# Kernel optimization log

Measured on AMD Instinct MI355X. Metric: run time of the kernel, lower is better.

## Reference

```python
import jax, jax.numpy as jnp
import numpy as np

B, T, E, D, OUT = 128, 64, 256, 256, 1  # batch, timesteps, encoder_hidden, decoder_hidden, out_feats


def setup_inputs() -> dict:
    key = jax.random.key(0)
    ks = jax.random.split(key, 14)
    s = 0.05
    return {
        "input_encoded": jax.random.normal(ks[0], (B, T, E), jnp.float32),
        "y_history": jax.random.normal(ks[1], (B, T - 1, OUT), jnp.float32),
        # attn_layer: Linear(2D+E -> E), Tanh, Linear(E -> 1)
        "W_a1": jax.random.normal(ks[2], (E, 2 * D + E), jnp.float32) * s,
        "b_a1": jax.random.normal(ks[3], (E,), jnp.float32) * s,
        "W_a2": jax.random.normal(ks[4], (1, E), jnp.float32) * s,
        "b_a2": jax.random.normal(ks[5], (1,), jnp.float32) * s,
        # fc: Linear(E + out_feats -> out_feats)
        "W_fc": jax.random.normal(ks[6], (OUT, E + OUT), jnp.float32) * s,
        "b_fc": jax.random.normal(ks[7], (OUT,), jnp.float32) * s,
        # LSTM(input_size=out_feats, hidden_size=D), gate order i,f,g,o
        "W_ih": jax.random.normal(ks[8], (4 * D, OUT), jnp.float32) * s,
        "W_hh": jax.random.normal(ks[9], (4 * D, D), jnp.float32) * s,
        "b_ih": jax.random.normal(ks[10], (4 * D,), jnp.float32) * s,
        "b_hh": jax.random.normal(ks[11], (4 * D,), jnp.float32) * s,
        # fc_final: Linear(D + E -> 2) (probabilistic=True)
        "W_ff": jax.random.normal(ks[12], (2, D + E), jnp.float32) * s,
        "b_ff": jax.random.normal(ks[13], (2,), jnp.float32) * s,
    }


def reference(input_encoded, y_history, W_a1, b_a1, W_a2, b_a2, W_fc, b_fc,
              W_ih, W_hh, b_ih, b_hh, W_ff, b_ff):
    Bn, Tn, En = input_encoded.shape
    Dn = W_hh.shape[1]

    def step(carry, y_t):
        h, c, _ = carry  # h, c: [B, D]
        # concat(hidden, cell, enc) broadcast over the T encoder positions -> [B, T, 2D+E]
        feats = jnp.concatenate([
            jnp.broadcast_to(h[:, None, :], (Bn, Tn, Dn)),
            jnp.broadcast_to(c[:, None, :], (Bn, Tn, Dn)),
            input_encoded,
        ], axis=2)
        scores = jnp.tanh(feats @ W_a1.T + b_a1) @ W_a2.T + b_a2  # [B, T, 1]
        attn = jax.nn.softmax(scores[..., 0], axis=1)              # [B, T]
        context = jnp.einsum('bt,bte->be', attn, input_encoded)   # [B, E]
        y_tilde = jnp.concatenate([context, y_t], axis=1) @ W_fc.T + b_fc  # [B, 1]
        # single LSTM step, PyTorch gate order (i, f, g, o)
        gates = y_tilde @ W_ih.T + b_ih + h @ W_hh.T + b_hh       # [B, 4D]
        i, f, g, o = jnp.split(gates, 4, axis=1)
        c_new = jax.nn.sigmoid(f) * c + jax.nn.sigmoid(i) * jnp.tanh(g)
        h_new = jax.nn.sigmoid(o) * jnp.tanh(c_new)
        return (h_new, c_new, context), None

    h0 = jnp.zeros((Bn, Dn), input_encoded.dtype)
    c0 = jnp.zeros((Bn, Dn), input_encoded.dtype)
    ctx0 = jnp.zeros((Bn, En), input_encoded.dtype)
    # data_integration=True: loop runs T-1 steps over y_history
    (h, c, context), _ = jax.lax.scan(step, (h0, c0, ctx0), jnp.swapaxes(y_history, 0, 1))
    return jnp.concatenate([h, context], axis=1) @ W_ff.T + b_ff  # [B, 2]
```

## Files before the change

kernel.cpp:

```cpp
#include <hip/hip_runtime.h>
#include <math.h>

#define BATCH 128
#define TENC  64
#define NSTEP 63

#define OFF_WA1ET  0
#define OFF_EPT    65536
#define OFF_PKH    2162688
#define OFF_SX     2359296
#define OFF_HX     2375680
#define OFF_FLAGS  2408448

typedef __attribute__((ext_vector_type(8))) _Float16 h8_t;
typedef __attribute__((ext_vector_type(2))) _Float16 h2_t;

#if defined(__has_builtin)
#if __has_builtin(__builtin_amdgcn_fdot2)
#define FDOT2(a, b, c) __builtin_amdgcn_fdot2((a), (b), (c), false)
#endif
#endif
#ifndef FDOT2
#define FDOT2(a, b, c) ((c) + (float)(a)[0] * (float)(b)[0] + (float)(a)[1] * (float)(b)[1])
#endif

__device__ __forceinline__ h2_t h2of(h8_t v, int i) {
    h2_t r = {v[2 * i], v[2 * i + 1]};
    return r;
}
__device__ __forceinline__ float ftanh(float x) {
    x = fminf(15.f, fmaxf(-15.f, x));
    float e = __expf(2.f * x);
    return (e - 1.f) * __builtin_amdgcn_rcpf(e + 1.f);
}
__device__ __forceinline__ float fsig(float x) {
    return __builtin_amdgcn_rcpf(1.f + __expf(-x));
}
__device__ __forceinline__ unsigned pack_hc(float h, float c) {
    unsigned short hu = __builtin_bit_cast(unsigned short, (_Float16)h);
    unsigned short cu = __builtin_bit_cast(unsigned short, (_Float16)c);
    return (unsigned)hu | ((unsigned)cu << 16);
}

__global__ void pack_weights(const float* __restrict__ Wa1,
                             const float* __restrict__ Whh,
                             float* __restrict__ ws) {
    int idx = blockIdx.x * blockDim.x + threadIdx.x;
    _Float16* PKH = (_Float16*)(ws + OFF_PKH);
    if (idx < 131072) {
        int m = idx & 7, j7 = (idx >> 3) & 127, it = (idx >> 10) & 3;
        int seg = (idx >> 12) & 1, kc = (idx >> 13) & 7, hp = (idx >> 16) & 1;
        int owner = seg ? (1 - hp) : hp;
        int idx256 = kc * 32 + it * 8 + m;
        int k = (idx256 < 128) ? owner * 128 + idx256
                               : 256 + owner * 128 + (idx256 - 128);
        int j = hp * 128 + j7;
        PKH[idx] = (_Float16)Wa1[j * 768 + k];
    } else if (idx < 393216) {
        int n = idx - 131072;
        int m = n & 7, qp = (n >> 3) & 511, kh = (n >> 12) & 1, kk = (n >> 13) & 15, h1 = n >> 17;
        int q = ((qp >> 7) << 8) + h1 * 128 + (qp & 127);
        int k = kh * 128 + kk * 8 + m;
        PKH[131072 + n] = (_Float16)Whh[q * 256 + k];
    } else if (idx < 458752) {
        int n = idx - 393216;
        int k = n >> 8, j = n & 255;
        ws[OFF_WA1ET + n] = Wa1[j * 768 + 512 + k];
    }
}

__global__ void zero_flags(float* __restrict__ ws) {
    unsigned* f = (unsigned*)(ws + OFF_FLAGS);
    f[threadIdx.x] = 0u;
}

__global__ void enc_proj_kernel(const float* __restrict__ enc,
                                const float* __restrict__ ba1,
                                float* __restrict__ ws) {
    __shared__ float smem[8448];
    const int b  = blockIdx.x >> 1;
    const int th = blockIdx.x & 1;
    const int t0 = th * 32;
    const int tid = threadIdx.x;

    const float* encb = enc + (b * TENC + t0) * 256;
    for (int c = 0; c < 32; ++c) smem[c * 256 + tid] = encb[c * 256 + tid];
    __syncthreads();

    const int w = tid >> 6, l = tid & 63;
    float acc[8][4];
    #pragma unroll
    for (int a = 0; a < 8; ++a)
        #pragma unroll
        for (int c = 0; c < 4; ++c) acc[a][c] = 0.f;

    const float4* WT = (const float4*)(ws + OFF_WA1ET);
    for (int k = 0; k < 256; ++k) {
        float4 wv = WT[k * 64 + l];
        #pragma unroll
        for (int tt = 0; tt < 8; ++tt) {
            float e = smem[(w * 8 + tt) * 256 + k];
            acc[tt][0] += e * wv.x; acc[tt][1] += e * wv.y;
            acc[tt][2] += e * wv.z; acc[tt][3] += e * wv.w;
        }
    }
    float4 bb = ((const float4*)ba1)[l];
    __syncthreads();
    #pragma unroll
    for (int tt = 0; tt < 8; ++tt) {
        smem[(4 * l + 0) * 33 + w * 8 + tt] = acc[tt][0] + bb.x;
        smem[(4 * l + 1) * 33 + w * 8 + tt] = acc[tt][1] + bb.y;
        smem[(4 * l + 2) * 33 + w * 8 + tt] = acc[tt][2] + bb.z;
        smem[(4 * l + 3) * 33 + w * 8 + tt] = acc[tt][3] + bb.w;
    }
    __syncthreads();
    float* EPT = ws + OFF_EPT + b * 16384;
    for (int c = 0; c < 32; ++c) {
        int i = c * 256 + tid;
        int j = i >> 5, t5 = i & 31;
        EPT[j * 64 + t0 + t5] = smem[j * 33 + t5];
    }
}

__global__ __launch_bounds__(1024, 4) void decoder_main(
    const float* __restrict__ enc, const float* __restrict__ yhist,
    const float* __restrict__ Wa2,
    const float* __restrict__ Wfc, const float* __restrict__ bfc,
    const float* __restrict__ wih, const float* __restrict__ bih,
    const float* __restrict__ bhh,
    const float* __restrict__ Wff, const float* __restrict__ bff,
    float* __restrict__ ws, float* __restrict__ out) {

    __shared__ float hc[512];
    __shared__ _Float16 hcf16[512] __attribute__((aligned(16)));
    __shared__ float z[128];
    __shared__ float red1[1024];
    __shared__ float red2[1024];
    __shared__ float g2[1024];
    __shared__ float attnw[64];
    __shared__ float encw[64];
    __shared__ float sownl[64];
    __shared__ float wa2s[128];
    __shared__ float ys[64];
    __shared__ h8_t  wc[6144] __attribute__((aligned(16)));
    __shared__ float epl[8192];

    const int bid  = blockIdx.x;
    const int b    = bid & 127;
    const int h1   = bid >> 7;
    const int tid  = threadIdx.x;
    const int lane = tid & 63;
    const int wv   = tid >> 6;

    const _Float16* PKH = (const _Float16*)(ws + OFF_PKH);

    const float* EPTb = ws + OFF_EPT + b * 16384 + h1 * 8192;
    const float* encb = enc + b * 16384;
    #pragma unroll
    for (int i = 0; i < 8; ++i) epl[i * 1024 + tid] = EPTb[i * 1024 + tid];
    const h8_t* PKGown = (const h8_t*)(PKH + 131072) + h1 * 16384;
    #pragma unroll
    for (int kk = 0; kk < 6; ++kk) wc[kk * 1024 + tid] = PKGown[kk * 1024 + tid];
    if (tid < 512) { hc[tid] = 0.f; hcf16[tid] = (_Float16)0.f; }
    if (tid < 128) wa2s[tid] = Wa2[h1 * 128 + tid];
    if (tid < NSTEP) ys[tid] = yhist[b * NSTEP + tid];
    const float bfc0  = bfc[0];
    const float wfc_y = Wfc[256];
    float wii = 0.f, wif = 0.f, wig = 0.f, wio = 0.f;
    float bsi = 0.f, bsf = 0.f, bsg = 0.f, bso = 0.f;
    if (tid < 128) {
        const int q0 = h1 * 128 + tid;
        wii = wih[q0];       bsi = bih[q0]       + bhh[q0];
        wif = wih[256 + q0]; bsf = bih[256 + q0] + bhh[256 + q0];
        wig = wih[512 + q0]; bsg = bih[512 + q0] + bhh[512 + q0];
        wio = wih[768 + q0]; bso = bih[768 + q0] + bhh[768 + q0];
    }
    {
        const int t = tid >> 4, cch = tid & 15;
        float p = 0.f;
        #pragma unroll
        for (int i = 0; i < 16; ++i)
            p += encb[t * 256 + cch * 16 + i] * Wfc[cch * 16 + i];
        red1[t * 16 + cch] = p;
    }
    __syncthreads();
    if (tid < 64) {
        float s = 0.f;
        #pragma unroll
        for (int c = 0; c < 16; ++c) s += red1[tid * 16 + c];
        encw[tid] = s;
    }
    __syncthreads();

    const int kc = tid >> 7, j7 = tid & 127;
    const h8_t* W1 = (const h8_t*)PKH + h1 * 8192 + kc * 1024 + j7;
    const _Float16* hb_own  = hcf16 + ((kc < 4) ? h1 * 128 + kc * 32
                                                : 256 + h1 * 128 + (kc - 4) * 32);
    const _Float16* hb_peer = hcf16 + ((kc < 4) ? (1 - h1) * 128 + kc * 32
                                                : 256 + (1 - h1) * 128 + (kc - 4) * 32);
    const int kh = tid >> 9, qp = tid & 511;
    const h8_t* W4 = PKGown + kh * 512 + qp;
    const _Float16* hgk = hcf16 + kh * 128;

    float*    SXown  = ws + OFF_SX + (b * 2 + h1) * 64;
    float*    SXpeer = ws + OFF_SX + (b * 2 + (1 - h1)) * 64;
    unsigned* HXown  = (unsigned*)(ws + OFF_HX) + (b * 2 + h1) * 128;
    unsigned* HXpeer = (unsigned*)(ws + OFF_HX) + (b * 2 + (1 - h1)) * 128;
    unsigned* FLGown  = (unsigned*)(ws + OFF_FLAGS) + (b * 2 + h1) * 2;
    unsigned* FLGpeer = (unsigned*)(ws + OFF_FLAGS) + (b * 2 + (1 - h1)) * 2;

    for (int step = 0; step < NSTEP; ++step) {
        const unsigned tgt = (unsigned)(step + 1);
        float a0 = 0.f, a1 = 0.f;
        #pragma unroll
        for (int it = 0; it < 4; ++it) {
            h8_t w  = W1[it * 128];
            h8_t hv = *(const h8_t*)(hb_own + it * 8);
            a0 = FDOT2(h2of(w, 0), h2of(hv, 0), a0);
            a1 = FDOT2(h2of(w, 1), h2of(hv, 1), a1);
            a0 = FDOT2(h2of(w, 2), h2of(hv, 2), a0);
            a1 = FDOT2(h2of(w, 3), h2of(hv, 3), a1);
        }
        if (tid == 0 && step > 0) {
            while (atomicAdd(&FLGpeer[0], 0u) < (unsigned)step) { __builtin_amdgcn_s_sleep(1); }
        }
        __syncthreads();
        if (tid < 128 && step > 0) {
            unsigned u = atomicAdd(&HXpeer[tid], 0u);
            _Float16 hv16 = __builtin_bit_cast(_Float16, (unsigned short)(u & 0xffffu));
            _Float16 cv16 = __builtin_bit_cast(_Float16, (unsigned short)(u >> 16));
            const int ih = (1 - h1) * 128 + tid;
            hcf16[ih] = hv16; hcf16[256 + ih] = cv16;
            hc[ih] = (float)hv16;
        }
        __syncthreads();
        #pragma unroll
        for (int it = 0; it < 4; ++it) {
            h8_t w  = W1[512 + it * 128];
            h8_t hv = *(const h8_t*)(hb_peer + it * 8);
            a0 = FDOT2(h2of(w, 0), h2of(hv, 0), a0);
            a1 = FDOT2(h2of(w, 1), h2of(hv, 1), a1);
            a0 = FDOT2(h2of(w, 2), h2of(hv, 2), a0);
            a1 = FDOT2(h2of(w, 3), h2of(hv, 3), a1);
        }
        red1[kc * 128 + j7] = a0 + a1;
        __syncthreads();
        if (tid < 128) {
            float s = red1[tid];
            #pragma unroll
            for (int c = 1; c < 8; ++c) s += red1[c * 128 + tid];
            z[tid] = s;
        }
        __syncthreads();

        {
            const int jc = tid >> 6;
            float partial = 0.f;
            #pragma unroll
            for (int jj = 0; jj < 8; ++jj) {
                const int j = jc * 8 + jj;
                float v = epl[j * 64 + lane] + z[j];
                partial += ftanh(v) * wa2s[j];
            }
            red2[jc * 64 + lane] = partial;
        }
        __syncthreads();

        if (wv == 0) {
            float s = 0.f;
            #pragma unroll
            for (int w2 = 0; w2 < 16; ++w2) s += red2[w2 * 64 + lane];
            sownl[lane] = s;
            atomicExch(&SXown[lane], s);
            asm volatile("s_waitcnt vmcnt(0)" ::: "memory");
            if (lane == 0) atomicExch(&FLGown[1], tgt);
        }
        float g0 = 0.f, g1 = 0.f;
        #pragma unroll
        for (int kk = 0; kk < 6; ++kk) {
            h8_t w  = wc[kk * 1024 + tid];
            h8_t hv = *(const h8_t*)(hgk + kk * 8);
            g0 = FDOT2(h2of(w, 0), h2of(hv, 0), g0);
            g1 = FDOT2(h2of(w, 1), h2of(hv, 1), g1);
            g0 = FDOT2(h2of(w, 2), h2of(hv, 2), g0);
            g1 = FDOT2(h2of(w, 3), h2of(hv, 3), g1);
        }
        #pragma unroll 5
        for (int kk = 6; kk < 16; ++kk) {
            h8_t w  = W4[kk * 1024];
            h8_t hv = *(const h8_t*)(hgk + kk * 8);
            g0 = FDOT2(h2of(w, 0), h2of(hv, 0), g0);
            g1 = FDOT2(h2of(w, 1), h2of(hv, 1), g1);
            g0 = FDOT2(h2of(w, 2), h2of(hv, 2), g0);
            g1 = FDOT2(h2of(w, 3), h2of(hv, 3), g1);
        }
        g2[tid] = g0 + g1;
        if (tid == 0) {
            while (atomicAdd(&FLGpeer[1], 0u) < tgt) { __builtin_amdgcn_s_sleep(1); }
        }
        __syncthreads();

        if (tid < 128) {
            float sp = atomicAdd(&SXpeer[lane], 0.f);
            float s  = sownl[lane] + sp;
            float m = s;
            #pragma unroll
            for (int d = 32; d >= 1; d >>= 1) m = fmaxf(m, __shfl_xor(m, d));
            float e = __expf(s - m);
            float su = e;
            #pragma unroll
            for (int d = 32; d >= 1; d >>= 1) su += __shfl_xor(su, d);
            float a = e * __builtin_amdgcn_rcpf(su);
            if (wv == 0) attnw[lane] = a;
            float yp = a * encw[lane];
            #pragma unroll
            for (int d = 32; d >= 1; d >>= 1) yp += __shfl_xor(yp, d);
            const float ytil = yp + wfc_y * ys[step] + bfc0;

            float gi = g2[tid]       + g2[512 + tid] + ytil * wii + bsi;
            float gf = g2[128 + tid] + g2[640 + tid] + ytil * wif + bsf;
            float gg = g2[256 + tid] + g2[768 + tid] + ytil * wig + bsg;
            float go = g2[384 + tid] + g2[896 + tid] + ytil * wio + bso;
            const int ih = h1 * 128 + tid;
            float co = hc[256 + ih];
            float cn = fsig(gf) * co + fsig(gi) * ftanh(gg);
            float hn = fsig(go) * ftanh(cn);
            hc[ih] = hn; hc[256 + ih] = cn;
            hcf16[ih] = (_Float16)hn; hcf16[256 + ih] = (_Float16)cn;
            atomicExch(&HXown[tid], pack_hc(hn, cn));
        }
        __syncthreads();
        if (tid == 0) atomicExch(&FLGown[0], tgt);
    }

    if (tid == 0) {
        while (atomicAdd(&FLGpeer[0], 0u) < (unsigned)NSTEP) { __builtin_amdgcn_s_sleep(1); }
    }
    __syncthreads();
    if (tid < 128) {
        unsigned u = atomicAdd(&HXpeer[tid], 0u);
        _Float16 hv16 = __builtin_bit_cast(_Float16, (unsigned short)(u & 0xffffu));
        hc[(1 - h1) * 128 + tid] = (float)hv16;
    }
    __syncthreads();

    if (h1 == 0) {
        if (tid < 256) {
            float cv = 0.f;
            #pragma unroll 8
            for (int t = 0; t < TENC; ++t)
                cv += attnw[t] * encb[t * 256 + tid];
            red1[tid] = cv;
        }
        __syncthreads();
        if (wv < 2) {
            float partial = 0.f;
            #pragma unroll
            for (int qq = 0; qq < 8; ++qq) {
                const int e2 = qq * 64 + lane;
                float v = (e2 < 256) ? hc[e2] : red1[e2 - 256];
                partial += v * Wff[wv * 512 + e2];
            }
            #pragma unroll
            for (int d = 32; d >= 1; d >>= 1) partial += __shfl_xor(partial, d);
            if (lane == 0) out[b * 2 + wv] = partial + bff[wv];
        }
    }
}

extern "C" void kernel_launch(void* const* d_in, const int* in_sizes, int n_in,
                              void* d_out, int out_size, void* d_ws, size_t ws_size,
                              hipStream_t stream) {
    const float* enc = (const float*)d_in[0];
    const float* yh  = (const float*)d_in[1];
    const float* Wa1 = (const float*)d_in[2];
    const float* ba1 = (const float*)d_in[3];
    const float* Wa2 = (const float*)d_in[4];
    const float* Wfc = (const float*)d_in[6];
    const float* bfc = (const float*)d_in[7];
    const float* Wih = (const float*)d_in[8];
    const float* Whh = (const float*)d_in[9];
    const float* bih = (const float*)d_in[10];
    const float* bhh = (const float*)d_in[11];
    const float* Wff = (const float*)d_in[12];
    const float* bff = (const float*)d_in[13];
    float* ws  = (float*)d_ws;
    float* out = (float*)d_out;

    hipLaunchKernelGGL(pack_weights, dim3(1792), dim3(256), 0, stream, Wa1, Whh, ws);
    hipLaunchKernelGGL(zero_flags, dim3(1), dim3(512), 0, stream, ws);
    hipLaunchKernelGGL(enc_proj_kernel, dim3(256), dim3(256), 0, stream, enc, ba1, ws);
    hipLaunchKernelGGL(decoder_main, dim3(256), dim3(1024), 0, stream,
                       enc, yh, Wa2, Wfc, bfc, Wih, bih, bhh, Wff, bff, ws, out);
}
```

Before: 408.4 us.

## Warp-specialize decoder step: split attention and LSTM gate work across thread halves

The per-step block-wide barriers are replaced by warp specialization. Threads 0-511 compute the attention projection, scores and softmax plus the LSTM cell update, while threads 512-1023 receive the peer's h/c and compute the recurrent gate matvec (two rows per thread, more weights cached in LDS). The halves coordinate through LDS atomic counters with spin-waits instead of __syncthreads, so the gate GEMV can overlap the attention chain. This adds spin-wait and memory-ordering complexity, and each half now does twice the per-thread work.

```diff
diff --git a/kernel.cpp b/kernel.cpp
--- a/kernel.cpp
+++ b/kernel.cpp
@@ -11,6 +11,11 @@
 #define OFF_SX     2359296
 #define OFF_HX     2375680
 #define OFF_FLAGS  2408448
+
+#define SF 0
+#define AF 1
+#define CF 2
+#define GF 3
 
 typedef __attribute__((ext_vector_type(8))) _Float16 h8_t;
 typedef __attribute__((ext_vector_type(2))) _Float16 h2_t;
@@ -41,6 +46,8 @@
     unsigned short cu = __builtin_bit_cast(unsigned short, (_Float16)c);
     return (unsigned)hu | ((unsigned)cu << 16);
 }
+#define FENCE() asm volatile("" ::: "memory")
+#define LGKM0() asm volatile("s_waitcnt lgkmcnt(0)" ::: "memory")
 
 __global__ void pack_weights(const float* __restrict__ Wa1,
                              const float* __restrict__ Whh,
@@ -48,10 +55,10 @@
     int idx = blockIdx.x * blockDim.x + threadIdx.x;
     _Float16* PKH = (_Float16*)(ws + OFF_PKH);
     if (idx < 131072) {
-        int m = idx & 7, j7 = (idx >> 3) & 127, it = (idx >> 10) & 3;
-        int seg = (idx >> 12) & 1, kc = (idx >> 13) & 7, hp = (idx >> 16) & 1;
+        int m = idx & 7, j7 = (idx >> 3) & 127, it = (idx >> 10) & 7;
+        int seg = (idx >> 13) & 1, kc = (idx >> 14) & 3, hp = (idx >> 16) & 1;
         int owner = seg ? (1 - hp) : hp;
-        int idx256 = kc * 32 + it * 8 + m;
+        int idx256 = kc * 64 + it * 8 + m;
         int k = (idx256 < 128) ? owner * 128 + idx256
                                : 256 + owner * 128 + (idx256 - 128);
         int j = hp * 128 + j7;
@@ -133,37 +140,52 @@
 
     __shared__ float hc[512];
     __shared__ _Float16 hcf16[512] __attribute__((aligned(16)));
-    __shared__ float z[128];
-    __shared__ float red1[1024];
-    __shared__ float red2[1024];
-    __shared__ float g2[1024];
+    __shared__ float red1[512];
+    __shared__ float red2[512];
+    __shared__ float g2[512];
     __shared__ float attnw[64];
     __shared__ float encw[64];
-    __shared__ float sownl[64];
     __shared__ float wa2s[128];
     __shared__ float ys[64];
-    __shared__ h8_t  wc[6144] __attribute__((aligned(16)));
+    __shared__ unsigned fl[4];
+    __shared__ h8_t  wc[7168] __attribute__((aligned(16)));
     __shared__ float epl[8192];
 
     const int bid  = blockIdx.x;
     const int b    = bid & 127;
     const int h1   = bid >> 7;
     const int tid  = threadIdx.x;
-    const int lane = tid & 63;
-    const int wv   = tid >> 6;
 
     const _Float16* PKH = (const _Float16*)(ws + OFF_PKH);
-
     const float* EPTb = ws + OFF_EPT + b * 16384 + h1 * 8192;
     const float* encb = enc + b * 16384;
+
+    if (tid < 512) { hc[tid] = 0.f; hcf16[tid] = (_Float16)0.f; }
+    if (tid < 128) wa2s[tid] = Wa2[h1 * 128 + tid];
+    if (tid < NSTEP) ys[tid] = yhist[b * NSTEP + tid];
+    if (tid < 4) fl[tid] = 0u;
+    {
+        float* scr = (float*)wc;
+        const int t = tid >> 4, cch = tid & 15;
+        float p = 0.f;
+        #pragma unroll
+        for (int i = 0; i < 16; ++i)
+            p += encb[t * 256 + cch * 16 + i] * Wfc[cch * 16 + i];
+        scr[t * 16 + cch] = p;
+    }
+    __syncthreads();
+    if (tid < 64) {
+        float s = 0.f;
+        #pragma unroll
+        for (int c = 0; c < 16; ++c) s += ((float*)wc)[tid * 16 + c];
+        encw[tid] = s;
+    }
+    __syncthreads();
     #pragma unroll
     for (int i = 0; i < 8; ++i) epl[i * 1024 + tid] = EPTb[i * 1024 + tid];
     const h8_t* PKGown = (const h8_t*)(PKH + 131072) + h1 * 16384;
     #pragma unroll
-    for (int kk = 0; kk < 6; ++kk) wc[kk * 1024 + tid] = PKGown[kk * 1024 + tid];
-    if (tid < 512) { hc[tid] = 0.f; hcf16[tid] = (_Float16)0.f; }
-    if (tid < 128) wa2s[tid] = Wa2[h1 * 128 + tid];
-    if (tid < NSTEP) ys[tid] = yhist[b * NSTEP + tid];
+    for (int kk = 0; kk < 7; ++kk) wc[kk * 1024 + tid] = PKGown[kk * 1024 + tid];
     const float bfc0  = bfc[0];
     const float wfc_y = Wfc[256];
     float wii = 0.f, wif = 0.f, wig = 0.f, wio = 0.f;
@@ -175,32 +197,16 @@
         wig = wih[512 + q0]; bsg = bih[512 + q0] + bhh[512 + q0];
         wio = wih[768 + q0]; bso = bih[768 + q0] + bhh[768 + q0];
     }
-    {
-        const int t = tid >> 4, cch = tid & 15;
-        float p = 0.f;
-        #pragma unroll
-        for (int i = 0; i < 16; ++i)
-            p += encb[t * 256 + cch * 16 + i] * Wfc[cch * 16 + i];
-        red1[t * 16 + cch] = p;
-    }
-    __syncthreads();
-    if (tid < 64) {
-        float s = 0.f;
-        #pragma unroll
-        for (int c = 0; c < 16; ++c) s += red1[tid * 16 + c];
-        encw[tid] = s;
-    }
-    __syncthreads();
-
-    const int kc = tid >> 7, j7 = tid & 127;
-    const h8_t* W1 = (const h8_t*)PKH + h1 * 8192 + kc * 1024 + j7;
-    const _Float16* hb_own  = hcf16 + ((kc < 4) ? h1 * 128 + kc * 32
-                                                : 256 + h1 * 128 + (kc - 4) * 32);
-    const _Float16* hb_peer = hcf16 + ((kc < 4) ? (1 - h1) * 128 + kc * 32
-                                                : 256 + (1 - h1) * 128 + (kc - 4) * 32);
-    const int kh = tid >> 9, qp = tid & 511;
-    const h8_t* W4 = PKGown + kh * 512 + qp;
-    const _Float16* hgk = hcf16 + kh * 128;
+    __syncthreads();
+
+    const int j7 = tid & 127, kc = (tid >> 7) & 3;
+    const h8_t* W1a = (const h8_t*)PKH + ((h1 * 4 + kc) * 2 + 0) * 1024 + j7;
+    const h8_t* W1b = W1a + 1024;
+    const _Float16* hb_own  = hcf16 + ((kc < 2) ? h1 * 128 + kc * 64
+                                                : 256 + h1 * 128 + (kc - 2) * 64);
+    const _Float16* hb_peer = hcf16 + ((kc < 2) ? (1 - h1) * 128 + kc * 64
+                                                : 256 + (1 - h1) * 128 + (kc - 2) * 64);
+    const h8_t* W4 = PKGown + (tid - 512);
 
     float*    SXown  = ws + OFF_SX + (b * 2 + h1) * 64;
     float*    SXpeer = ws + OFF_SX + (b * 2 + (1 - h1)) * 64;
@@ -211,123 +217,146 @@
 
     for (int step = 0; step < NSTEP; ++step) {
         const unsigned tgt = (unsigned)(step + 1);
-        float a0 = 0.f, a1 = 0.f;
-        #pragma unroll
-        for (int it = 0; it < 4; ++it) {
-            h8_t w  = W1[it * 128];
-            h8_t hv = *(const h8_t*)(hb_own + it * 8);
-            a0 = FDOT2(h2of(w, 0), h2of(hv, 0), a0);
-            a1 = FDOT2(h2of(w, 1), h2of(hv, 1), a1);
-            a0 = FDOT2(h2of(w, 2), h2of(hv, 2), a0);
-            a1 = FDOT2(h2of(w, 3), h2of(hv, 3), a1);
-        }
-        if (tid == 0 && step > 0) {
-            while (atomicAdd(&FLGpeer[0], 0u) < (unsigned)step) { __builtin_amdgcn_s_sleep(1); }
-        }
-        __syncthreads();
-        if (tid < 128 && step > 0) {
-            unsigned u = atomicAdd(&HXpeer[tid], 0u);
-            _Float16 hv16 = __builtin_bit_cast(_Float16, (unsigned short)(u & 0xffffu));
-            _Float16 cv16 = __builtin_bit_cast(_Float16, (unsigned short)(u >> 16));
-            const int ih = (1 - h1) * 128 + tid;
-            hcf16[ih] = hv16; hcf16[256 + ih] = cv16;
-            hc[ih] = (float)hv16;
-        }
-        __syncthreads();
-        #pragma unroll
-        for (int it = 0; it < 4; ++it) {
-            h8_t w  = W1[512 + it * 128];
-            h8_t hv = *(const h8_t*)(hb_peer + it * 8);
-            a0 = FDOT2(h2of(w, 0), h2of(hv, 0), a0);
-            a1 = FDOT2(h2of(w, 1), h2of(hv, 1), a1);
-            a0 = FDOT2(h2of(w, 2), h2of(hv, 2), a0);
-            a1 = FDOT2(h2of(w, 3), h2of(hv, 3), a1);
-        }
-        red1[kc * 128 + j7] = a0 + a1;
-        __syncthreads();
-        if (tid < 128) {
-            float s = red1[tid];
+        if (tid < 512) {
+            float a0 = 0.f, a1 = 0.f;
+            #pragma unroll 4
+            for (int it = 0; it < 8; ++it) {
+                h8_t w  = W1a[it * 128];
+                h8_t hv = *(const h8_t*)(hb_own + it * 8);
+                a0 = FDOT2(h2of(w, 0), h2of(hv, 0), a0);
+                a1 = FDOT2(h2of(w, 1), h2of(hv, 1), a1);
+                a0 = FDOT2(h2of(w, 2), h2of(hv, 2), a0);
+                a1 = FDOT2(h2of(w, 3), h2of(hv, 3), a1);
+            }
+            if (step) {
+                while (atomicAdd(&fl[SF], 0u) < 2u * (unsigned)step)
+                    __builtin_amdgcn_s_sleep(1);
+                FENCE();
+            }
+            #pragma unroll 4
+            for (int it = 0; it < 8; ++it) {
+                h8_t w  = W1b[it * 128];
+                h8_t hv = *(const h8_t*)(hb_peer + it * 8);
+                a0 = FDOT2(h2of(w, 0), h2of(hv, 0), a0);
+                a1 = FDOT2(h2of(w, 1), h2of(hv, 1), a1);
+                a0 = FDOT2(h2of(w, 2), h2of(hv, 2), a0);
+                a1 = FDOT2(h2of(w, 3), h2of(hv, 3), a1);
+            }
+            red1[kc * 128 + j7] = a0 + a1;
+            LGKM0();
+            if ((tid & 63) == 0) atomicAdd(&fl[AF], 1u);
+            while (atomicAdd(&fl[AF], 0u) < 8u * tgt) __builtin_amdgcn_s_sleep(1);
+            FENCE();
+            {
+                const int jc = tid >> 6, lane = tid & 63;
+                float partial = 0.f;
+                #pragma unroll
+                for (int jj = 0; jj < 16; ++jj) {
+                    const int j = jc * 16 + jj;
+                    float zj = red1[j] + red1[128 + j] + red1[256 + j] + red1[384 + j];
+                    float v = epl[j * 64 + lane] + zj;
+                    partial += ftanh(v) * wa2s[j];
+                }
+                red2[jc * 64 + lane] = partial;
+            }
+            LGKM0();
+            if ((tid & 63) == 0) atomicAdd(&fl[CF], 1u);
+            if (tid < 128) {
+                const int lane = tid & 63;
+                while (atomicAdd(&fl[CF], 0u) < 8u * tgt) __builtin_amdgcn_s_sleep(1);
+                FENCE();
+                float s = 0.f;
+                #pragma unroll
+                for (int jc2 = 0; jc2 < 8; ++jc2) s += red2[jc2 * 64 + lane];
+                if (tid < 64) {
+                    atomicExch(&SXown[lane], s);
+                    asm volatile("s_waitcnt vmcnt(0)" ::: "memory");
+                    if (lane == 0) atomicExch(&FLGown[1], tgt);
+                }
+                while (atomicAdd(&FLGpeer[1], 0u) < tgt) __builtin_amdgcn_s_sleep(1);
+                FENCE();
+                s += atomicAdd(&SXpeer[lane], 0.f);
+                float m = s;
+                #pragma unroll
+                for (int d = 32; d >= 1; d >>= 1) m = fmaxf(m, __shfl_xor(m, d));
+                float e = __expf(s - m);
+                float su = e;
+                #pragma unroll
+                for (int d = 32; d >= 1; d >>= 1) su += __shfl_xor(su, d);
+                float a = e * __builtin_amdgcn_rcpf(su);
+                if (tid < 64) attnw[lane] = a;
+                float yp = a * encw[lane];
+                #pragma unroll
+                for (int d = 32; d >= 1; d >>= 1) yp += __shfl_xor(yp, d);
+                const float ytil = yp + wfc_y * ys[step] + bfc0;
+                while (atomicAdd(&fl[GF], 0u) < 8u * tgt) __builtin_amdgcn_s_sleep(1);
+                FENCE();
+                float gi = g2[tid]       + ytil * wii + bsi;
+                float gf = g2[128 + tid] + ytil * wif + bsf;
+                float gg = g2[256 + tid] + ytil * wig + bsg;
+                float go = g2[384 + tid] + ytil * wio + bso;
+                const int ih = h1 * 128 + tid;
+                float co = hc[256 + ih];
+                float cn = fsig(gf) * co + fsig(gi) * ftanh(gg);
+                float hn = fsig(go) * ftanh(cn);
+                hc[ih] = hn; hc[256 + ih] = cn;
+                hcf16[ih] = (_Float16)hn; hcf16[256 + ih] = (_Float16)cn;
+                atomicExch(&HXown[tid], pack_hc(hn, cn));
+            }
+        } else {
+            const int u2 = tid - 512;
+            if (step) {
+                if (u2 < 128) {
+                    while (atomicAdd(&FLGpeer[0], 0u) < (unsigned)step)
+                        __builtin_amdgcn_s_sleep(1);
+                    FENCE();
+                    unsigned uu = atomicAdd(&HXpeer[u2], 0u);
+                    _Float16 hv16 = __builtin_bit_cast(_Float16, (unsigned short)(uu & 0xffffu));
+                    _Float16 cv16 = __builtin_bit_cast(_Float16, (unsigned short)(uu >> 16));
+                    const int ih = (1 - h1) * 128 + u2;
+                    hcf16[ih] = hv16; hcf16[256 + ih] = cv16;
+                    hc[ih] = (float)hv16;
+                    LGKM0();
+                    if ((u2 & 63) == 0) atomicAdd(&fl[SF], 1u);
+                }
+                while (atomicAdd(&fl[SF], 0u) < 2u * (unsigned)step)
+                    __builtin_amdgcn_s_sleep(1);
+                FENCE();
+            }
+            float ga = 0.f, gb = 0.f;
             #pragma unroll
-            for (int c = 1; c < 8; ++c) s += red1[c * 128 + tid];
-            z[tid] = s;
-        }
-        __syncthreads();
-
-        {
-            const int jc = tid >> 6;
-            float partial = 0.f;
-            #pragma unroll
-            for (int jj = 0; jj < 8; ++jj) {
-                const int j = jc * 8 + jj;
-                float v = epl[j * 64 + lane] + z[j];
-                partial += ftanh(v) * wa2s[j];
-            }
-            red2[jc * 64 + lane] = partial;
-        }
-        __syncthreads();
-
-        if (wv == 0) {
-            float s = 0.f;
-            #pragma unroll
-            for (int w2 = 0; w2 < 16; ++w2) s += red2[w2 * 64 + lane];
-            sownl[lane] = s;
-            atomicExch(&SXown[lane], s);
-            asm volatile("s_waitcnt vmcnt(0)" ::: "memory");
-            if (lane == 0) atomicExch(&FLGown[1], tgt);
-        }
-        float g0 = 0.f, g1 = 0.f;
-        #pragma unroll
-        for (int kk = 0; kk < 6; ++kk) {
-            h8_t w  = wc[kk * 1024 + tid];
-            h8_t hv = *(const h8_t*)(hgk + kk * 8);
-            g0 = FDOT2(h2of(w, 0), h2of(hv, 0), g0);
-            g1 = FDOT2(h2of(w, 1), h2of(hv, 1), g1);
-            g0 = FDOT2(h2of(w, 2), h2of(hv, 2), g0);
-            g1 = FDOT2(h2of(w, 3), h2of(hv, 3), g1);
-        }
-        #pragma unroll 5
-        for (int kk = 6; kk < 16; ++kk) {
-            h8_t w  = W4[kk * 1024];
-            h8_t hv = *(const h8_t*)(hgk + kk * 8);
-            g0 = FDOT2(h2of(w, 0), h2of(hv, 0), g0);
-            g1 = FDOT2(h2of(w, 1), h2of(hv, 1), g1);
-            g0 = FDOT2(h2of(w, 2), h2of(hv, 2), g0);
-            g1 = FDOT2(h2of(w, 3), h2of(hv, 3), g1);
-        }
-        g2[tid] = g0 + g1;
-        if (tid == 0) {
-            while (atomicAdd(&FLGpeer[1], 0u) < tgt) { __builtin_amdgcn_s_sleep(1); }
-        }
-        __syncthreads();
-
-        if (tid < 128) {
-            float sp = atomicAdd(&SXpeer[lane], 0.f);
-            float s  = sownl[lane] + sp;
-            float m = s;
-            #pragma unroll
-            for (int d = 32; d >= 1; d >>= 1) m = fmaxf(m, __shfl_xor(m, d));
-            float e = __expf(s - m);
-            float su = e;
-            #pragma unroll
-            for (int d = 32; d >= 1; d >>= 1) su += __shfl_xor(su, d);
-            float a = e * __builtin_amdgcn_rcpf(su);
-            if (wv == 0) attnw[lane] = a;
-            float yp = a * encw[lane];
-            #pragma unroll
-            for (int d = 32; d >= 1; d >>= 1) yp += __shfl_xor(yp, d);
-            const float ytil = yp + wfc_y * ys[step] + bfc0;
-
-            float gi = g2[tid]       + g2[512 + tid] + ytil * wii + bsi;
-            float gf = g2[128 + tid] + g2[640 + tid] + ytil * wif + bsf;
-            float gg = g2[256 + tid] + g2[768 + tid] + ytil * wig + bsg;
-            float go = g2[384 + tid] + g2[896 + tid] + ytil * wio + bso;
-            const int ih = h1 * 128 + tid;
-            float co = hc[256 + ih];
-            float cn = fsig(gf) * co + fsig(gi) * ftanh(gg);
-            float hn = fsig(go) * ftanh(cn);
-            hc[ih] = hn; hc[256 + ih] = cn;
-            hcf16[ih] = (_Float16)hn; hcf16[256 + ih] = (_Float16)cn;
-            atomicExch(&HXown[tid], pack_hc(hn, cn));
+            for (int kk = 0; kk < 7; ++kk) {
+                h8_t w0  = wc[kk * 1024 + u2];
+                h8_t w1  = wc[kk * 1024 + 512 + u2];
+                h8_t hv0 = *(const h8_t*)(hcf16 + kk * 8);
+                h8_t hv1 = *(const h8_t*)(hcf16 + 128 + kk * 8);
+                ga = FDOT2(h2of(w0, 0), h2of(hv0, 0), ga);
+                gb = FDOT2(h2of(w1, 0), h2of(hv1, 0), gb);
+                ga = FDOT2(h2of(w0, 1), h2of(hv0, 1), ga);
+                gb = FDOT2(h2of(w1, 1), h2of(hv1, 1), gb);
+                ga = FDOT2(h2of(w0, 2), h2of(hv0, 2), ga);
+                gb = FDOT2(h2of(w1, 2), h2of(hv1, 2), gb);
+                ga = FDOT2(h2of(w0, 3), h2of(hv0, 3), ga);
+                gb = FDOT2(h2of(w1, 3), h2of(hv1, 3), gb);
+            }
+            #pragma unroll 3
+            for (int kk = 7; kk < 16; ++kk) {
+                h8_t w0  = W4[kk * 1024];
+                h8_t w1  = W4[kk * 1024 + 512];
+                h8_t hv0 = *(const h8_t*)(hcf16 + kk * 8);
+                h8_t hv1 = *(const h8_t*)(hcf16 + 128 + kk * 8);
+                ga = FDOT2(h2of(w0, 0), h2of(hv0, 0), ga);
+                gb = FDOT2(h2of(w1, 0), h2of(hv1, 0), gb);
+                ga = FDOT2(h2of(w0, 1), h2of(hv0, 1), ga);
+                gb = FDOT2(h2of(w1, 1), h2of(hv1, 1), gb);
+                ga = FDOT2(h2of(w0, 2), h2of(hv0, 2), ga);
+                gb = FDOT2(h2of(w1, 2), h2of(hv1, 2), gb);
+                ga = FDOT2(h2of(w0, 3), h2of(hv0, 3), ga);
+                gb = FDOT2(h2of(w1, 3), h2of(hv1, 3), gb);
+            }
+            g2[u2] = ga + gb;
+            LGKM0();
+            if ((u2 & 63) == 0) atomicAdd(&fl[GF], 1u);
         }
         __syncthreads();
         if (tid == 0) atomicExch(&FLGown[0], tgt);
@@ -338,8 +367,8 @@
     }
     __syncthreads();
     if (tid < 128) {
-        unsigned u = atomicAdd(&HXpeer[tid], 0u);
-        _Float16 hv16 = __builtin_bit_cast(_Float16, (unsigned short)(u & 0xffffu));
+        unsigned uu = atomicAdd(&HXpeer[tid], 0u);
+        _Float16 hv16 = __builtin_bit_cast(_Float16, (unsigned short)(uu & 0xffffu));
         hc[(1 - h1) * 128 + tid] = (float)hv16;
     }
     __syncthreads();
@@ -353,17 +382,18 @@
             red1[tid] = cv;
         }
         __syncthreads();
-        if (wv < 2) {
+        if (tid < 128) {
+            const int wvv = tid >> 6, lane = tid & 63;
             float partial = 0.f;
             #pragma unroll
             for (int qq = 0; qq < 8; ++qq) {
                 const int e2 = qq * 64 + lane;
                 float v = (e2 < 256) ? hc[e2] : red1[e2 - 256];
-                partial += v * Wff[wv * 512 + e2];
+                partial += v * Wff[wvv * 512 + e2];
             }
             #pragma unroll
             for (int d = 32; d >= 1; d >>= 1) partial += __shfl_xor(partial, d);
-            if (lane == 0) out[b * 2 + wv] = partial + bff[wv];
+            if (lane == 0) out[b * 2 + wvv] = partial + bff[wvv];
         }
     }
 }
```

After: 398.8 us. 2.4% less time.
